# Kernel optimization log

Hardware: AMD Instinct MI355X
Metric: run time of the kernel (lower is better)

## Reference

```python
import jax, jax.numpy as jnp
import numpy as np

B, S, D, H = 2, 2048, 768, 12
DK = D // H

def setup_inputs() -> dict:
    key = jax.random.key(0)
    ks = jax.random.split(key, 11)
    sc = 0.02
    inp = {
        'Q': jax.random.normal(ks[0], (B, S, D), jnp.float32),
        'K': jax.random.normal(ks[1], (B, S, D), jnp.float32),
        'V': jax.random.normal(ks[2], (B, S, D), jnp.float32),
        # causal mask, broadcastable over batch and heads (1 = keep, 0 = mask)
        'mask': jnp.tril(jnp.ones((S, S), jnp.int32))[None, None, :, :],
        'Wq': jax.random.normal(ks[3], (D, D), jnp.float32) * sc,
        'bq': jax.random.normal(ks[4], (D,), jnp.float32) * sc,
        'Wk': jax.random.normal(ks[5], (D, D), jnp.float32) * sc,
        'bk': jax.random.normal(ks[6], (D,), jnp.float32) * sc,
        'Wv': jax.random.normal(ks[7], (D, D), jnp.float32) * sc,
        'bv': jax.random.normal(ks[8], (D,), jnp.float32) * sc,
        'Wo': jax.random.normal(ks[9], (D, D), jnp.float32) * sc,
        'bo': jax.random.normal(ks[10], (D,), jnp.float32) * sc,
    }
    return inp

def _split_heads(x):
    # [B,S,D] -> [B,H,S,DK]
    return x.reshape(B, S, H, DK).transpose(0, 2, 1, 3)

def reference(Q, K, V, mask, Wq, bq, Wk, bk, Wv, bv, Wo, bo):
    # torch Linear: y = x @ W.T + b
    q = _split_heads(Q @ Wq.T + bq)
    k = _split_heads(K @ Wk.T + bk)
    v = _split_heads(V @ Wv.T + bv)
    scores = jnp.einsum('bhqd,bhkd->bhqk', q, k) / jnp.sqrt(jnp.float32(DK))
    scores = jnp.where(mask == 0, jnp.float32(-1e9), scores)
    attn = jax.nn.softmax(scores, axis=-1)
    out = jnp.einsum('bhqk,bhkd->bhqd', attn, v)  # [B,H,S,DK]
    out = out.transpose(0, 2, 1, 3).reshape(B, S, D)
    return out @ Wo.T + bo
```

## Files before the change

kernel.cpp:

```cpp
#include <hip/hip_runtime.h>
#include <hip/hip_bf16.h>

#define H_  12
#define S_  2048
#define D_  768
#define DK_ 64

typedef __bf16 bf16x8 __attribute__((ext_vector_type(8)));
typedef __bf16 bf16x4 __attribute__((ext_vector_type(4)));
typedef short  short4v __attribute__((ext_vector_type(4)));
typedef float  f32x4  __attribute__((ext_vector_type(4)));

#define QSCALE 0.1803368801111137f

__device__ inline float exp2_fast(float x) {
  return __builtin_amdgcn_exp2f(x);
}

__device__ inline f32x4 mfma_bf16(bf16x8 a, bf16x8 b, f32x4 c) {
  return __builtin_amdgcn_mfma_f32_16x16x32_bf16(a, b, c, 0, 0, 0);
}

__device__ inline f32x4 mfma16(bf16x4 a, bf16x4 b, f32x4 c) {
#if __has_builtin(__builtin_amdgcn_mfma_f32_16x16x16bf16_1k)
  short4v as = __builtin_bit_cast(short4v, a);
  short4v bs = __builtin_bit_cast(short4v, b);
  return __builtin_amdgcn_mfma_f32_16x16x16bf16_1k(as, bs, c, 0, 0, 0);
#else
  asm("s_nop 1\n\tv_mfma_f32_16x16x16_bf16 %0, %1, %2, %0"
      : "+v"(c) : "v"(a), "v"(b));
  return c;
#endif
}

__device__ inline void gload16(const void* g, void* l) {
  __builtin_amdgcn_global_load_lds(
      (const __attribute__((address_space(1))) void*)g,
      (__attribute__((address_space(3))) void*)l, 16, 0, 0);
}

__device__ inline bf16x8 cvt2bf16(f32x4 a, f32x4 b) {
  bf16x8 r;
  r[0] = (__bf16)a[0]; r[1] = (__bf16)a[1];
  r[2] = (__bf16)a[2]; r[3] = (__bf16)a[3];
  r[4] = (__bf16)b[0]; r[5] = (__bf16)b[1];
  r[6] = (__bf16)b[2]; r[7] = (__bf16)b[3];
  return r;
}

__global__ __launch_bounds__(256)
void conv_w(const float* __restrict__ Wq, const float* __restrict__ Wk,
            const float* __restrict__ Wv, const float* __restrict__ Wo,
            __hip_bfloat16* __restrict__ out)
{
  const int i8 = blockIdx.x * 256 + threadIdx.x;
  const int mat = i8 / 73728;
  const int off = (i8 - mat * 73728) * 8;
  const float* src = (mat == 0) ? Wq : (mat == 1) ? Wk : (mat == 2) ? Wv : Wo;
  f32x4 a = *(const f32x4*)(src + off);
  f32x4 b = *(const f32x4*)(src + off + 4);
  *(bf16x8*)(out + (size_t)mat * 589824 + off) = cvt2bf16(a, b);
}

__global__ __launch_bounds__(256, 3)
void qkv_proj(const float* __restrict__ Q, const float* __restrict__ K,
              const float* __restrict__ V,
              const __hip_bfloat16* __restrict__ Wb,
              const float* __restrict__ bq, const float* __restrict__ bk,
              const float* __restrict__ bv,
              __hip_bfloat16* __restrict__ q_ws,
              __hip_bfloat16* __restrict__ k_ws,
              __hip_bfloat16* __restrict__ vT_ws)
{
  __shared__ alignas(16) __hip_bfloat16 Ald[128 * 32];
  __shared__ alignas(16) __hip_bfloat16 Bld[128 * 32];

  const int z = blockIdx.z;
  const float* X    = (z == 0) ? Q  : (z == 1) ? K  : V;
  const float* bias = (z == 0) ? bq : (z == 1) ? bk : bv;
  const __hip_bfloat16* Wz = Wb + (size_t)z * 589824;
  __hip_bfloat16* out = (z == 0) ? q_ws : (z == 1) ? k_ws : vT_ws;
  const bool vmode = (z == 2);
  const float osc = (z == 0) ? QSCALE : 1.0f;

  const int t    = threadIdx.x;
  const int w    = t >> 6;
  const int lane = t & 63;
  const int l15  = lane & 15;
  const int quad = lane >> 4;
  const int m0 = blockIdx.x * 128;
  const int n0 = blockIdx.y * 128;
  const int wm = (w >> 1) * 64;
  const int wn = (w & 1) * 64;

  const f32x4 fzero = {0.f, 0.f, 0.f, 0.f};
  f32x4 acc[4][4];
#pragma unroll
  for (int i = 0; i < 4; ++i)
#pragma unroll
    for (int j = 0; j < 4; ++j) acc[i][j] = fzero;

  const int ar = t >> 2, ac = t & 3;
  const int sw = ac ^ ((ar >> 1) & 3);
  const float* As0 = X + (size_t)(m0 + ar) * D_ + ac * 8;
  const float* As1 = X + (size_t)(m0 + ar + 64) * D_ + ac * 8;
  __hip_bfloat16* Aw0 = &Ald[((ar)      * 4 + sw) * 8];
  __hip_bfloat16* Aw1 = &Ald[((ar + 64) * 4 + sw) * 8];

  const int bp = (t & 3) ^ (((t >> 2) >> 1) & 3);
  const __hip_bfloat16* Bs0 = Wz + (size_t)(n0 + (t >> 2)) * D_ + bp * 8;
  const __hip_bfloat16* Bs1 = Wz + (size_t)(n0 + (t >> 2) + 64) * D_ + bp * 8;
  __hip_bfloat16* Bd0 = &Bld[t * 8];
  __hip_bfloat16* Bd1 = &Bld[(t + 256) * 8];

  int agrn[4], bgrn[4];
#pragma unroll
  for (int i = 0; i < 4; ++i) {
    int row = wm + 16 * i + l15;
    agrn[i] = (row * 4 + (quad ^ ((row >> 1) & 3))) * 8;
    row = wn + 16 * i + l15;
    bgrn[i] = (row * 4 + (quad ^ ((row >> 1) & 3))) * 8;
  }

  f32x4 a00 = *(const f32x4*)As0, a01 = *(const f32x4*)(As0 + 4);
  f32x4 a10 = *(const f32x4*)As1, a11 = *(const f32x4*)(As1 + 4);

  for (int k0 = 0; k0 < D_; k0 += 32) {
    *(bf16x8*)Aw0 = cvt2bf16(a00, a01);
    *(bf16x8*)Aw1 = cvt2bf16(a10, a11);
    gload16(Bs0 + k0, Bd0);
    gload16(Bs1 + k0, Bd1);
    __syncthreads();

    const int kn = k0 + 32;
    if (kn < D_) {
      a00 = *(const f32x4*)(As0 + kn); a01 = *(const f32x4*)(As0 + kn + 4);
      a10 = *(const f32x4*)(As1 + kn); a11 = *(const f32x4*)(As1 + kn + 4);
    }

    bf16x8 af[4], bfr[4];
#pragma unroll
    for (int i = 0; i < 4; ++i) af[i]  = *(const bf16x8*)&Ald[agrn[i]];
#pragma unroll
    for (int j = 0; j < 4; ++j) bfr[j] = *(const bf16x8*)&Bld[bgrn[j]];
#pragma unroll
    for (int i = 0; i < 4; ++i)
#pragma unroll
      for (int j = 0; j < 4; ++j)
        acc[i][j] = mfma_bf16(af[i], bfr[j], acc[i][j]);
    __syncthreads();
  }

#pragma unroll
  for (int j = 0; j < 4; ++j) {
    const int n_g = n0 + wn + 16 * j + l15;
    const float bv = bias[n_g];
    const int hh = n_g >> 6, dk = n_g & (DK_ - 1);
#pragma unroll
    for (int i = 0; i < 4; ++i) {
      const int mbase = m0 + wm + 16 * i + quad * 4;
#pragma unroll
      for (int r = 0; r < 4; ++r) {
        const int m_g = mbase + r;
        const int bb = m_g >> 11, ss = m_g & (S_ - 1);
        const float vout = (acc[i][j][r] + bv) * osc;
        size_t idx;
        if (vmode)
          idx = (((size_t)(bb * H_ + hh)) * DK_ + dk) * S_ + ss;
        else
          idx = (((size_t)(bb * H_ + hh)) * S_ + ss) * DK_ + dk;
        out[idx] = __float2bfloat16(vout);
      }
    }
  }
}

__global__ __launch_bounds__(256, 4)
void o_proj(const __hip_bfloat16* __restrict__ Xb,
            const __hip_bfloat16* __restrict__ Wob,
            const float* __restrict__ bias,
            float* __restrict__ outf)
{
  __shared__ alignas(16) __hip_bfloat16 Ald[64 * 32];
  __shared__ alignas(16) __hip_bfloat16 Bld[128 * 32];

  const int t    = threadIdx.x;
  const int w    = t >> 6;
  const int lane = t & 63;
  const int l15  = lane & 15;
  const int quad = lane >> 4;
  const int m0 = blockIdx.x * 64;
  const int n0 = blockIdx.y * 128;
  const int wm = (w >> 1) * 32;
  const int wn = (w & 1) * 64;

  const f32x4 fzero = {0.f, 0.f, 0.f, 0.f};
  f32x4 acc[2][4];
#pragma unroll
  for (int i = 0; i < 2; ++i)
#pragma unroll
    for (int j = 0; j < 4; ++j) acc[i][j] = fzero;

  const int ap = (t & 3) ^ (((t >> 2) >> 1) & 3);
  const __hip_bfloat16* As  = Xb  + (size_t)(m0 + (t >> 2)) * D_ + ap * 8;
  const __hip_bfloat16* Bs0 = Wob + (size_t)(n0 + (t >> 2)) * D_ + ap * 8;
  const __hip_bfloat16* Bs1 = Wob + (size_t)(n0 + (t >> 2) + 64) * D_ + ap * 8;
  __hip_bfloat16* Ad  = &Ald[t * 8];
  __hip_bfloat16* Bd0 = &Bld[t * 8];
  __hip_bfloat16* Bd1 = &Bld[(t + 256) * 8];

  int agrn[2], bgrn[4];
#pragma unroll
  for (int i = 0; i < 2; ++i) {
    const int row = wm + 16 * i + l15;
    agrn[i] = (row * 4 + (quad ^ ((row >> 1) & 3))) * 8;
  }
#pragma unroll
  for (int j = 0; j < 4; ++j) {
    const int row = wn + 16 * j + l15;
    bgrn[j] = (row * 4 + (quad ^ ((row >> 1) & 3))) * 8;
  }

  for (int k0 = 0; k0 < D_; k0 += 32) {
    gload16(As + k0, Ad);
    gload16(Bs0 + k0, Bd0);
    gload16(Bs1 + k0, Bd1);
    __syncthreads();

    bf16x8 af[2], bfr[4];
#pragma unroll
    for (int i = 0; i < 2; ++i) af[i]  = *(const bf16x8*)&Ald[agrn[i]];
#pragma unroll
    for (int j = 0; j < 4; ++j) bfr[j] = *(const bf16x8*)&Bld[bgrn[j]];
#pragma unroll
    for (int i = 0; i < 2; ++i)
#pragma unroll
      for (int j = 0; j < 4; ++j)
        acc[i][j] = mfma_bf16(af[i], bfr[j], acc[i][j]);
    __syncthreads();
  }

#pragma unroll
  for (int j = 0; j < 4; ++j) {
    const int n_g = n0 + wn + 16 * j + l15;
    const float bv = bias[n_g];
#pragma unroll
    for (int i = 0; i < 2; ++i) {
      const int mbase = m0 + wm + 16 * i + quad * 4;
#pragma unroll
      for (int r = 0; r < 4; ++r)
        outf[(size_t)(mbase + r) * D_ + n_g] = acc[i][j][r] + bv;
    }
  }
}

__global__ __launch_bounds__(256, 4)
void flash_attn(const __hip_bfloat16* __restrict__ q_ws,
                const __hip_bfloat16* __restrict__ k_ws,
                const __hip_bfloat16* __restrict__ vT_ws,
                __hip_bfloat16* __restrict__ o_ws)
{
  __shared__ alignas(16) __hip_bfloat16 Kld[128][72];
  __shared__ alignas(16) __hip_bfloat16 Vld[64][136];

  const int t = threadIdx.x, w = t >> 6, lane = t & 63;
  const int l15 = lane & 15, quad = lane >> 4;
  const int bh = blockIdx.y;
  const int b = bh / H_, h = bh % H_;
  const int x = blockIdx.x;
  const int tLo = x, tHi = 63 - x;
  const int myTile = (w < 2) ? tLo : tHi;
  const int qbase = myTile * 32 + 16 * (w & 1);
  const int qg = qbase + l15;
  const int myNkt = (myTile >> 2) + 1;
  const int nktT  = (tHi >> 2) + 1;
  const size_t hbase = (size_t)bh * S_ * DK_;
  const size_t vtb   = (size_t)bh * DK_ * S_;

  bf16x8 qf[2];
#pragma unroll
  for (int kk = 0; kk < 2; ++kk)
    qf[kk] = *(const bf16x8*)(q_ws + hbase + (size_t)qg * DK_ + kk * 32 + quad * 8);

  const f32x4 fzero = {0.f, 0.f, 0.f, 0.f};
  f32x4 accO[4];
#pragma unroll
  for (int jd = 0; jd < 4; ++jd) accO[jd] = fzero;
  float mI = -1.0e30f, lI = 0.f;

  const int tr = t >> 3, kg = t & 7;
  const int tv = t >> 4, vg = t & 15;
  const __hip_bfloat16* Kbase = k_ws + hbase + (size_t)tr * DK_ + kg * 8;
  const __hip_bfloat16* Vbase = vT_ws + vtb + (size_t)tv * S_ + vg * 8;

  bf16x8 rK[4], rV[4];
#pragma unroll
  for (int it = 0; it < 4; ++it) {
    rK[it] = *(const bf16x8*)(Kbase + (size_t)(32 * it) * DK_);
    rV[it] = *(const bf16x8*)(Vbase + (size_t)(16 * it) * S_);
  }

  for (int kt = 0; kt < nktT; ++kt) {
#pragma unroll
    for (int it = 0; it < 4; ++it) {
      *(bf16x8*)&Kld[32 * it + tr][kg * 8] = rK[it];
      *(bf16x8*)&Vld[16 * it + tv][vg * 8] = rV[it];
    }
    __syncthreads();

    if (kt + 1 < nktT) {
      const int k0n = (kt + 1) * 128;
#pragma unroll
      for (int it = 0; it < 4; ++it) {
        rK[it] = *(const bf16x8*)(Kbase + (size_t)(k0n + 32 * it) * DK_);
        rV[it] = *(const bf16x8*)(Vbase + (size_t)(16 * it) * S_ + k0n);
      }
    }

    if (kt < myNkt) {
      const int k0 = kt * 128;
      f32x4 st[8];
#pragma unroll
      for (int j = 0; j < 8; ++j) {
        bf16x8 kf0 = *(const bf16x8*)&Kld[16 * j + l15][quad * 8];
        bf16x8 kf1 = *(const bf16x8*)&Kld[16 * j + l15][32 + quad * 8];
        st[j] = mfma_bf16(kf0, qf[0], fzero);
        st[j] = mfma_bf16(kf1, qf[1], st[j]);
      }

      if (kt == myNkt - 1) {
#pragma unroll
        for (int j = 0; j < 8; ++j)
#pragma unroll
          for (int r = 0; r < 4; ++r) {
            const int kcg = k0 + 16 * j + quad * 4 + r;
            if (kcg > qg) st[j][r] = -1.0e9f;
          }
      }

      float tm = st[0][0];
#pragma unroll
      for (int j = 0; j < 8; ++j)
#pragma unroll
        for (int r = 0; r < 4; ++r) tm = fmaxf(tm, st[j][r]);
      tm = fmaxf(tm, __shfl_xor(tm, 16));
      tm = fmaxf(tm, __shfl_xor(tm, 32));

      const float mnew = fmaxf(mI, tm);
      const float al = exp2_fast(mI - mnew);
      mI = mnew;
      float rs = 0.f;
#pragma unroll
      for (int j = 0; j < 8; ++j)
#pragma unroll
        for (int r = 0; r < 4; ++r) {
          const float pv = exp2_fast(st[j][r] - mnew);
          st[j][r] = pv;
          rs += pv;
        }
      rs += __shfl_xor(rs, 16);
      rs += __shfl_xor(rs, 32);
      lI = lI * al + rs;
#pragma unroll
      for (int jd = 0; jd < 4; ++jd)
#pragma unroll
        for (int r = 0; r < 4; ++r) accO[jd][r] *= al;

      bf16x4 pb[8];
#pragma unroll
      for (int j = 0; j < 8; ++j) {
        pb[j][0] = (__bf16)st[j][0]; pb[j][1] = (__bf16)st[j][1];
        pb[j][2] = (__bf16)st[j][2]; pb[j][3] = (__bf16)st[j][3];
      }

#pragma unroll
      for (int jd = 0; jd < 4; ++jd)
#pragma unroll
        for (int j = 0; j < 8; ++j) {
          bf16x4 vf = *(const bf16x4*)&Vld[16 * jd + l15][16 * j + quad * 4];
          accO[jd] = mfma16(vf, pb[j], accO[jd]);
        }
    }
    __syncthreads();
  }

  const float inv = 1.f / lI;
#pragma unroll
  for (int jd = 0; jd < 4; ++jd) {
    bf16x4 ov;
#pragma unroll
    for (int r = 0; r < 4; ++r) ov[r] = (__bf16)(accO[jd][r] * inv);
    *(bf16x4*)(o_ws + ((size_t)b * S_ + qg) * D_ + h * DK_ + 16 * jd + quad * 4) = ov;
  }
}

extern "C" void kernel_launch(void* const* d_in, const int* in_sizes, int n_in,
                              void* d_out, int out_size, void* d_ws, size_t ws_size,
                              hipStream_t stream) {
  (void)in_sizes; (void)n_in; (void)out_size; (void)ws_size;
  const float* Q  = (const float*)d_in[0];
  const float* K  = (const float*)d_in[1];
  const float* V  = (const float*)d_in[2];
  const float* Wq = (const float*)d_in[4];
  const float* bq = (const float*)d_in[5];
  const float* Wk = (const float*)d_in[6];
  const float* bk = (const float*)d_in[7];
  const float* Wv = (const float*)d_in[8];
  const float* bv = (const float*)d_in[9];
  const float* Wo = (const float*)d_in[10];
  const float* bo = (const float*)d_in[11];
  float* out = (float*)d_out;

  const size_t WEL = (size_t)4 * 589824;
  const size_t NEL = (size_t)2 * S_ * D_;
  __hip_bfloat16* wb    = (__hip_bfloat16*)d_ws;
  __hip_bfloat16* q_ws  = wb + WEL;
  __hip_bfloat16* k_ws  = q_ws  + NEL;
  __hip_bfloat16* vT_ws = k_ws  + NEL;
  __hip_bfloat16* o_ws  = vT_ws + NEL;

  conv_w<<<1152, 256, 0, stream>>>(Wq, Wk, Wv, Wo, wb);
  qkv_proj<<<dim3(32, 6, 3), 256, 0, stream>>>(Q, K, V, wb, bq, bk, bv,
                                               q_ws, k_ws, vT_ws);
  flash_attn<<<dim3(32, 24), 256, 0, stream>>>(q_ws, k_ws, vT_ws, o_ws);
  o_proj<<<dim3(64, 6), 256, 0, stream>>>(o_ws, wb + (size_t)3 * 589824, bo, out);
}
```

Measured before the change: 207.3 us.

## Compute V projection transposed for coalesced V^T stores; remap attention block order

For the V projection, the X and weight tiles swap LDS buffers, so the MFMA produces the transposed product and lanes write consecutive sequence positions into the V^T layout, making those strided scatter stores coalesced. Flash attention moves to a 1D grid with a remapping that spreads heads across slots and staggers tile indices per group. The aim is better L2 locality and load balance across CUs. The remap adds index arithmetic and relies on the buffer swap being shape-symmetric, which holds because both tiles are 128x32.

```diff
diff --git a/kernel.cpp b/kernel.cpp
--- a/kernel.cpp
+++ b/kernel.cpp
@@ -93,6 +93,9 @@
   const int wm = (w >> 1) * 64;
   const int wn = (w & 1) * 64;
 
+  __hip_bfloat16* Xbuf = vmode ? Bld : Ald;
+  __hip_bfloat16* Wbuf = vmode ? Ald : Bld;
+
   const f32x4 fzero = {0.f, 0.f, 0.f, 0.f};
   f32x4 acc[4][4];
 #pragma unroll
@@ -104,14 +107,14 @@
   const int sw = ac ^ ((ar >> 1) & 3);
   const float* As0 = X + (size_t)(m0 + ar) * D_ + ac * 8;
   const float* As1 = X + (size_t)(m0 + ar + 64) * D_ + ac * 8;
-  __hip_bfloat16* Aw0 = &Ald[((ar)      * 4 + sw) * 8];
-  __hip_bfloat16* Aw1 = &Ald[((ar + 64) * 4 + sw) * 8];
+  __hip_bfloat16* Xw0 = &Xbuf[((ar)      * 4 + sw) * 8];
+  __hip_bfloat16* Xw1 = &Xbuf[((ar + 64) * 4 + sw) * 8];
 
   const int bp = (t & 3) ^ (((t >> 2) >> 1) & 3);
   const __hip_bfloat16* Bs0 = Wz + (size_t)(n0 + (t >> 2)) * D_ + bp * 8;
   const __hip_bfloat16* Bs1 = Wz + (size_t)(n0 + (t >> 2) + 64) * D_ + bp * 8;
-  __hip_bfloat16* Bd0 = &Bld[t * 8];
-  __hip_bfloat16* Bd1 = &Bld[(t + 256) * 8];
+  __hip_bfloat16* Wd0 = &Wbuf[t * 8];
+  __hip_bfloat16* Wd1 = &Wbuf[(t + 256) * 8];
 
   int agrn[4], bgrn[4];
 #pragma unroll
@@ -126,10 +129,10 @@
   f32x4 a10 = *(const f32x4*)As1, a11 = *(const f32x4*)(As1 + 4);
 
   for (int k0 = 0; k0 < D_; k0 += 32) {
-    *(bf16x8*)Aw0 = cvt2bf16(a00, a01);
-    *(bf16x8*)Aw1 = cvt2bf16(a10, a11);
-    gload16(Bs0 + k0, Bd0);
-    gload16(Bs1 + k0, Bd1);
+    *(bf16x8*)Xw0 = cvt2bf16(a00, a01);
+    *(bf16x8*)Xw1 = cvt2bf16(a10, a11);
+    gload16(Bs0 + k0, Wd0);
+    gload16(Bs1 + k0, Wd1);
     __syncthreads();
 
     const int kn = k0 + 32;
@@ -151,25 +154,41 @@
     __syncthreads();
   }
 
-#pragma unroll
-  for (int j = 0; j < 4; ++j) {
-    const int n_g = n0 + wn + 16 * j + l15;
-    const float bv = bias[n_g];
-    const int hh = n_g >> 6, dk = n_g & (DK_ - 1);
+  if (!vmode) {
+#pragma unroll
+    for (int j = 0; j < 4; ++j) {
+      const int n_g = n0 + wn + 16 * j + l15;
+      const float bv = bias[n_g];
+      const int hh = n_g >> 6, dk = n_g & (DK_ - 1);
+#pragma unroll
+      for (int i = 0; i < 4; ++i) {
+        const int mbase = m0 + wm + 16 * i + quad * 4;
+#pragma unroll
+        for (int r = 0; r < 4; ++r) {
+          const int m_g = mbase + r;
+          const int bb = m_g >> 11, ss = m_g & (S_ - 1);
+          const float vout = (acc[i][j][r] + bv) * osc;
+          out[(((size_t)(bb * H_ + hh)) * S_ + ss) * DK_ + dk] =
+              __float2bfloat16(vout);
+        }
+      }
+    }
+  } else {
 #pragma unroll
     for (int i = 0; i < 4; ++i) {
-      const int mbase = m0 + wm + 16 * i + quad * 4;
+      const int nbase = n0 + wm + 16 * i + quad * 4;
 #pragma unroll
       for (int r = 0; r < 4; ++r) {
-        const int m_g = mbase + r;
-        const int bb = m_g >> 11, ss = m_g & (S_ - 1);
-        const float vout = (acc[i][j][r] + bv) * osc;
-        size_t idx;
-        if (vmode)
-          idx = (((size_t)(bb * H_ + hh)) * DK_ + dk) * S_ + ss;
-        else
-          idx = (((size_t)(bb * H_ + hh)) * S_ + ss) * DK_ + dk;
-        out[idx] = __float2bfloat16(vout);
+        const int n_g = nbase + r;
+        const float bv = bias[n_g];
+        const int hh = n_g >> 6, dk = n_g & (DK_ - 1);
+#pragma unroll
+        for (int j = 0; j < 4; ++j) {
+          const int m_g = m0 + wn + 16 * j + l15;
+          const int bb = m_g >> 11, ss = m_g & (S_ - 1);
+          out[(((size_t)(bb * H_ + hh)) * DK_ + dk) * S_ + ss] =
+              __float2bfloat16(acc[i][j][r] + bv);
+        }
       }
     }
   }
@@ -265,9 +284,15 @@
 
   const int t = threadIdx.x, w = t >> 6, lane = t & 63;
   const int l15 = lane & 15, quad = lane >> 4;
-  const int bh = blockIdx.y;
+
+  const int id   = blockIdx.x;
+  const int slot = id & 7;
+  const int jj   = id >> 3;
+  const int grp  = jj >> 5;
+  const int bh   = slot + 8 * grp;
+  const int x    = ((jj & 31) + 13 * grp) & 31;
+
   const int b = bh / H_, h = bh % H_;
-  const int x = blockIdx.x;
   const int tLo = x, tHi = 63 - x;
   const int myTile = (w < 2) ? tLo : tHi;
   const int qbase = myTile * 32 + 16 * (w & 1);
@@ -422,6 +447,6 @@
   conv_w<<<1152, 256, 0, stream>>>(Wq, Wk, Wv, Wo, wb);
   qkv_proj<<<dim3(32, 6, 3), 256, 0, stream>>>(Q, K, V, wb, bq, bk, bv,
                                                q_ws, k_ws, vT_ws);
-  flash_attn<<<dim3(32, 24), 256, 0, stream>>>(q_ws, k_ws, vT_ws, o_ws);
+  flash_attn<<<768, 256, 0, stream>>>(q_ws, k_ws, vT_ws, o_ws);
   o_proj<<<dim3(64, 6), 256, 0, stream>>>(o_ws, wb + (size_t)3 * 589824, bo, out);
 }
```

Result: faster. 193.2 us (-6.8%).
